# Kernel tuning notes

Measured on AMD Instinct MI355X. Metric: run time of the kernel, lower is better.

## Reference

```python
import jax, jax.numpy as jnp
import numpy as np

B, N, F, UNITS = 8, 2048, 64, 64

def setup_inputs() -> dict:
    key = jax.random.key(0)
    ks = jax.random.split(key, 7)
    inputs = jax.random.normal(ks[0], (B, N, F), dtype=jnp.float32)
    Dynamic_L = jax.random.normal(ks[1], (B, N, N), dtype=jnp.float32)
    W = jax.random.uniform(ks[2], (B, N, N, 3), dtype=jnp.float32)
    Geo = jax.random.normal(ks[3], (N, N), dtype=jnp.float32)
    KL = jax.random.normal(ks[4], (N, N), dtype=jnp.float32)
    # Dense(Units, tanh) params (glorot-ish scale)
    Wd = jax.random.normal(ks[5], (F, UNITS), dtype=jnp.float32) / np.sqrt(F)
    bd = jnp.zeros((UNITS,), dtype=jnp.float32)
    return {"inputs": inputs, "Dynamic_L": Dynamic_L, "W": W,
            "Geo": Geo, "KL": KL, "Wd": Wd, "bd": bd}

def reference(inputs, Dynamic_L, W, Geo, KL, Wd, bd):
    # Weighted fusion of three N x N matrices; Geo/KL broadcast over batch.
    Fusion = Dynamic_L * W[..., 0] + Geo[None] * W[..., 1] + KL[None] * W[..., 2]  # [B,N,N]
    Fusion = jax.nn.softmax(Fusion, axis=-1)
    G1 = jnp.einsum('bnm,bmf->bnf', Fusion, inputs)  # graph matmul [B,N,F]
    return jnp.tanh(G1 @ Wd + bd)  # Dense(Units, tanh) -> [B,N,UNITS]
```

## Files before the change

### kernel.cpp

```cpp
#include <hip/hip_runtime.h>
#include <hip/hip_fp16.h>

#define Nn 2048
#define Ff 64
#define Uu 64
#define NT 512
#define NCH 4
#define G1S 68

typedef _Float16 f16x4 __attribute__((ext_vector_type(4)));
typedef _Float16 f16x8 __attribute__((ext_vector_type(8)));
typedef float    f32x4 __attribute__((ext_vector_type(4)));

#define MFMA32(a,b,c) __builtin_amdgcn_mfma_f32_16x16x32_f16(a,b,c,0,0,0)

#define OWS   65536
#define OINV  65664
#define SMSZ  65792

__global__ __launch_bounds__(256) void transposeX(const float* __restrict__ X,
                                                  _Float16* __restrict__ Xt) {
    __shared__ _Float16 tile[64][65];
    const int b = blockIdx.x, kt = blockIdx.y;
    #pragma unroll
    for (int i = 0; i < 16; ++i) {
        int e  = i * 256 + threadIdx.x;
        int kk = e >> 6, ff = e & 63;
        tile[ff][kk] = (_Float16)X[((size_t)b * Nn + kt * 64 + kk) * Ff + ff];
    }
    __syncthreads();
    #pragma unroll
    for (int i = 0; i < 16; ++i) {
        int e  = i * 256 + threadIdx.x;
        int ff = e >> 6, kk = e & 63;
        Xt[((size_t)b * Ff + ff) * Nn + kt * 64 + kk] = tile[ff][kk];
    }
}

#define ISSUE2(d0v,d1v,gv,kv,w00,w01,w02,w10,w11,w12, C, UR, H) {   \
    const size_t _o = (size_t)(UR) * Nn + ((size_t)(C) << 9)        \
                    + ((H) << 8) + (lane << 2);                     \
    d0v = *(const float4*)(dR0 + _o);                               \
    d1v = *(const float4*)(dR1 + _o);                               \
    gv  = *(const float4*)(gR + _o);                                \
    kv  = *(const float4*)(kR + _o);                                \
    w00 = *(const float4*)(wR0 + 3 * _o);                           \
    w01 = *(const float4*)(wR0 + 3 * _o + 4);                       \
    w02 = *(const float4*)(wR0 + 3 * _o + 8);                       \
    w10 = *(const float4*)(wR1 + 3 * _o);                           \
    w11 = *(const float4*)(wR1 + 3 * _o + 4);                       \
    w12 = *(const float4*)(wR1 + 3 * _o + 8);                       \
}

#define CONSUME2(d0v,d1v,gv,kv,w00,w01,w02,w10,w11,w12, P0B,P1B, UR, H) {       \
    const int _tr = row0 + (UR);                                                \
    float a0 = __expf(fminf(d0v.x*w00.x + gv.x*w00.y + kv.x*w00.z, 11.f));      \
    float a1 = __expf(fminf(d0v.y*w00.w + gv.y*w01.x + kv.y*w01.y, 11.f));      \
    float a2 = __expf(fminf(d0v.z*w01.z + gv.z*w01.w + kv.z*w02.x, 11.f));      \
    float a3 = __expf(fminf(d0v.w*w02.y + gv.w*w02.z + kv.w*w02.w, 11.f));      \
    float c0 = __expf(fminf(d1v.x*w10.x + gv.x*w10.y + kv.x*w10.z, 11.f));      \
    float c1 = __expf(fminf(d1v.y*w10.w + gv.y*w11.x + kv.y*w11.y, 11.f));      \
    float c2 = __expf(fminf(d1v.z*w11.z + gv.z*w11.w + kv.z*w12.x, 11.f));      \
    float c3 = __expf(fminf(d1v.w*w12.y + gv.w*w12.z + kv.w*w12.w, 11.f));      \
    f16x4 h0 = {(_Float16)a0, (_Float16)a1, (_Float16)a2, (_Float16)a3};        \
    f16x4 h1 = {(_Float16)c0, (_Float16)c1, (_Float16)c2, (_Float16)c3};        \
    rs0[UR] += (float)h0[0] + (float)h0[1] + (float)h0[2] + (float)h0[3];       \
    rs1[UR] += (float)h1[0] + (float)h1[1] + (float)h1[2] + (float)h1[3];       \
    const int _ba = (_tr * 1024 + ((H) << 9) + (lane << 3))                     \
                    ^ ((_tr & 7) << 4);                                         \
    *(f16x4*)((P0B) + _ba) = h0;                                                \
    *(f16x4*)((P1B) + _ba) = h1;                                                \
}

#define STAGE_CHUNK2(P0B, P1B, C) {                                              \
    ISSUE2(Ad0,Ad1,Agv,Akv,Aw00,Aw01,Aw02,Aw10,Aw11,Aw12, C, 0, 0);              \
    ISSUE2(Bd0,Bd1,Bgv,Bkv,Bw00,Bw01,Bw02,Bw10,Bw11,Bw12, C, 0, 1);              \
    CONSUME2(Ad0,Ad1,Agv,Akv,Aw00,Aw01,Aw02,Aw10,Aw11,Aw12, P0B,P1B, 0, 0);      \
    ISSUE2(Ad0,Ad1,Agv,Akv,Aw00,Aw01,Aw02,Aw10,Aw11,Aw12, C, 1, 0);              \
    CONSUME2(Bd0,Bd1,Bgv,Bkv,Bw00,Bw01,Bw02,Bw10,Bw11,Bw12, P0B,P1B, 0, 1);      \
    ISSUE2(Bd0,Bd1,Bgv,Bkv,Bw00,Bw01,Bw02,Bw10,Bw11,Bw12, C, 1, 1);              \
    CONSUME2(Ad0,Ad1,Agv,Akv,Aw00,Aw01,Aw02,Aw10,Aw11,Aw12, P0B,P1B, 1, 0);      \
    CONSUME2(Bd0,Bd1,Bgv,Bkv,Bw00,Bw01,Bw02,Bw10,Bw11,Bw12, P0B,P1B, 1, 1);      \
}

#define MFMA_PHASE2(PBUF, XC) {                                               \
    f16x8 p0 = *(const f16x8*)((XC));                                         \
    f16x8 p1 = *(const f16x8*)((XC) + 32);                                    \
    f16x8 p2 = *(const f16x8*)((XC) + 64);                                    \
    f16x8 p3 = *(const f16x8*)((XC) + 96);                                    \
    f16x8 p4 = *(const f16x8*)((XC) + 128);                                   \
    f16x8 p5 = *(const f16x8*)((XC) + 160);                                   \
    f16x8 p6 = *(const f16x8*)((XC) + 192);                                   \
    f16x8 p7 = *(const f16x8*)((XC) + 224);                                   \
    _Pragma("unroll")                                                         \
    for (int kk = 0; kk < 8; ++kk) {                                          \
        const int aa = r * 1024 + kk * 64 + kg * 16;                          \
        f16x8 af = *(const f16x8*)((PBUF) + (aa ^ ((r & 7) << 4)));           \
        f16x8 bv = (kk==0)?p0:(kk==1)?p1:(kk==2)?p2:(kk==3)?p3:               \
                   (kk==4)?p4:(kk==5)?p5:(kk==6)?p6:p7;                       \
        acc = MFMA32(af, bv, acc);                                            \
    }                                                                         \
    p0 = *(const f16x8*)((XC) + 256);                                         \
    p1 = *(const f16x8*)((XC) + 288);                                         \
    p2 = *(const f16x8*)((XC) + 320);                                         \
    p3 = *(const f16x8*)((XC) + 352);                                         \
    p4 = *(const f16x8*)((XC) + 384);                                         \
    p5 = *(const f16x8*)((XC) + 416);                                         \
    p6 = *(const f16x8*)((XC) + 448);                                         \
    p7 = *(const f16x8*)((XC) + 480);                                         \
    _Pragma("unroll")                                                         \
    for (int kk = 0; kk < 8; ++kk) {                                          \
        const int aa = r * 1024 + (kk + 8) * 64 + kg * 16;                    \
        f16x8 af = *(const f16x8*)((PBUF) + (aa ^ ((r & 7) << 4)));           \
        f16x8 bv = (kk==0)?p0:(kk==1)?p1:(kk==2)?p2:(kk==3)?p3:               \
                   (kk==4)?p4:(kk==5)?p5:(kk==6)?p6:p7;                       \
        acc = MFMA32(af, bv, acc);                                            \
    }                                                                         \
}

__global__ __launch_bounds__(NT, 4) void fused_gcn(
    const _Float16* __restrict__ Xt,
    const float* __restrict__ Dyn,
    const float* __restrict__ Wf,
    const float* __restrict__ Geo,
    const float* __restrict__ KLm,
    const float* __restrict__ Wd,
    const float* __restrict__ bdv,
    float* __restrict__ out)
{
    __shared__ __align__(16) char SM[SMSZ];

    const int t    = threadIdx.x;
    const int lane = t & 63;
    const int wid  = t >> 6;
    const int r    = lane & 15;
    const int kg   = lane >> 4;
    const int rg   = blockIdx.x & 127;
    const int pp   = blockIdx.x >> 7;
    const int n0   = rg << 4;
    const int b0   = pp * 2, b1 = pp * 2 + 1;
    const int row0 = wid << 1;

    const float* dR0 = Dyn + ((size_t)b0 * Nn + n0 + row0) * Nn;
    const float* dR1 = Dyn + ((size_t)b1 * Nn + n0 + row0) * Nn;
    const float* wR0 = Wf  + ((size_t)b0 * Nn + n0 + row0) * (size_t)Nn * 3;
    const float* wR1 = Wf  + ((size_t)b1 * Nn + n0 + row0) * (size_t)Nn * 3;
    const float* gR  = Geo + (size_t)(n0 + row0) * Nn;
    const float* kR  = KLm + (size_t)(n0 + row0) * Nn;

    const int bb = wid >> 2, ct = wid & 3;
    const _Float16* xwv = Xt + (size_t)(bb ? b1 : b0) * Ff * Nn
                        + (size_t)(ct * 16 + r) * Nn + (kg << 3);

    f32x4 acc = {0.f,0.f,0.f,0.f};
    float rs0[2] = {0.f,0.f}, rs1[2] = {0.f,0.f};
    float4 Ad0,Ad1,Agv,Akv,Aw00,Aw01,Aw02,Aw10,Aw11,Aw12;
    float4 Bd0,Bd1,Bgv,Bkv,Bw00,Bw01,Bw02,Bw10,Bw11,Bw12;

    STAGE_CHUNK2(SM, SM + 16384, 0);
    __syncthreads();

    #pragma unroll 1
    for (int c = 0; c < NCH; ++c) {
        const char* pb = SM + (c & 1) * 32768 + bb * 16384;
        MFMA_PHASE2(pb, xwv + ((size_t)c << 9));
        if (c + 1 < NCH) {
            char* bufn = SM + ((c + 1) & 1) * 32768;
            STAGE_CHUNK2(bufn, bufn + 16384, c + 1);
        }
        __syncthreads();
    }

    float* ws = (float*)(SM + OWS);
    #pragma unroll
    for (int i = 0; i < 2; ++i) {
        float v = rs0[i];
        v += __shfl_xor(v, 1, 64);  v += __shfl_xor(v, 2, 64);
        v += __shfl_xor(v, 4, 64);  v += __shfl_xor(v, 8, 64);
        v += __shfl_xor(v, 16, 64); v += __shfl_xor(v, 32, 64);
        float u = rs1[i];
        u += __shfl_xor(u, 1, 64);  u += __shfl_xor(u, 2, 64);
        u += __shfl_xor(u, 4, 64);  u += __shfl_xor(u, 8, 64);
        u += __shfl_xor(u, 16, 64); u += __shfl_xor(u, 32, 64);
        if (lane == 0) { ws[row0 + i] = v; ws[16 + row0 + i] = u; }
    }
    __syncthreads();
    float* inv = (float*)(SM + OINV);
    if (t < 32) inv[t] = 1.0f / ws[t];
    __syncthreads();

    float* g1a = (float*)SM;
    float* g1b = (float*)(SM + 4352);
    float* g1w = bb ? g1b : g1a;
    #pragma unroll
    for (int i = 0; i < 4; ++i) {
        const int ro = (kg << 2) + i;
        g1w[ro * G1S + ct * 16 + r] = acc[i] * inv[bb * 16 + ro];
    }
    __syncthreads();

    const int rw0 = (wid & 3) << 2;
    const float* gg = (bb ? g1b : g1a) + rw0 * G1S;
    const int ob = bb ? b1 : b0;
    float bias = bdv[lane];
    float o0 = bias, o1 = bias, o2 = bias, o3 = bias;
    #pragma unroll 4
    for (int f = 0; f < Ff; ++f) {
        float wdv = Wd[f * Uu + lane];
        o0 += gg[f] * wdv;           o1 += gg[G1S + f] * wdv;
        o2 += gg[2 * G1S + f] * wdv; o3 += gg[3 * G1S + f] * wdv;
    }
    float oo[4] = {o0, o1, o2, o3};
    #pragma unroll
    for (int i = 0; i < 4; ++i) {
        float x  = fminf(fmaxf(oo[i], -15.f), 15.f);
        float ex = __expf(2.f * x);
        out[((size_t)ob * Nn + n0 + rw0 + i) * Uu + lane] = (ex - 1.f) / (ex + 1.f);
    }
}

extern "C" void kernel_launch(void* const* d_in, const int* in_sizes, int n_in,
                              void* d_out, int out_size, void* d_ws, size_t ws_size,
                              hipStream_t stream) {
    const float* X   = (const float*)d_in[0];
    const float* Dyn = (const float*)d_in[1];
    const float* Wf  = (const float*)d_in[2];
    const float* Geo = (const float*)d_in[3];
    const float* KLm = (const float*)d_in[4];
    const float* Wd  = (const float*)d_in[5];
    const float* bdv = (const float*)d_in[6];
    float* out = (float*)d_out;

    _Float16* Xt = (_Float16*)d_ws;
    transposeX<<<dim3(8, Nn / 64), dim3(256), 0, stream>>>(X, Xt);
    fused_gcn<<<dim3(4 * 128), dim3(NT), 0, stream>>>(
        Xt, Dyn, Wf, Geo, KLm, Wd, bdv, out);
}
```

Measured before the change: 156.8 us.

## Halve rows per block to 8, shrink LDS, and use 256-thread blocks

Each block now covers 8 output rows per batch pair with 4 waves instead of 16 rows with 8 waves, which doubles the grid to 1024 blocks and roughly halves shared memory. Each wave computes two 16-column MFMA tiles, and rows 8-15 of each 16-row MFMA tile read from a zeroed LDS pad. The intent is higher occupancy and less register pressure during the load-heavy staging phase, with the loads split into separate per-batch A/B issues. The cost is half of each MFMA's work being wasted on zero rows, plus more per-block overhead.

```diff
diff --git a/kernel.cpp b/kernel.cpp
--- a/kernel.cpp
+++ b/kernel.cpp
@@ -4,7 +4,7 @@
 #define Nn 2048
 #define Ff 64
 #define Uu 64
-#define NT 512
+#define NT 256
 #define NCH 4
 #define G1S 68
 
@@ -14,9 +14,12 @@
 
 #define MFMA32(a,b,c) __builtin_amdgcn_mfma_f32_16x16x32_f16(a,b,c,0,0,0)
 
-#define OWS   65536
-#define OINV  65664
-#define SMSZ  65792
+#define OPB  0
+#define OZB  32768
+#define OWS  32896
+#define OINV 32960
+#define OG1  33024
+#define SMSZ 37376
 
 __global__ __launch_bounds__(256) void transposeX(const float* __restrict__ X,
                                                   _Float16* __restrict__ Xt) {
@@ -37,53 +40,69 @@
     }
 }
 
-#define ISSUE2(d0v,d1v,gv,kv,w00,w01,w02,w10,w11,w12, C, UR, H) {   \
+#define ISSUEA(C, UR, H) {                                          \
     const size_t _o = (size_t)(UR) * Nn + ((size_t)(C) << 9)        \
                     + ((H) << 8) + (lane << 2);                     \
-    d0v = *(const float4*)(dR0 + _o);                               \
-    d1v = *(const float4*)(dR1 + _o);                               \
-    gv  = *(const float4*)(gR + _o);                                \
-    kv  = *(const float4*)(kR + _o);                                \
-    w00 = *(const float4*)(wR0 + 3 * _o);                           \
-    w01 = *(const float4*)(wR0 + 3 * _o + 4);                       \
-    w02 = *(const float4*)(wR0 + 3 * _o + 8);                       \
-    w10 = *(const float4*)(wR1 + 3 * _o);                           \
-    w11 = *(const float4*)(wR1 + 3 * _o + 4);                       \
-    w12 = *(const float4*)(wR1 + 3 * _o + 8);                       \
-}
-
-#define CONSUME2(d0v,d1v,gv,kv,w00,w01,w02,w10,w11,w12, P0B,P1B, UR, H) {       \
+    Ad  = *(const float4*)(dR0 + _o);                               \
+    Aw0 = *(const float4*)(wR0 + 3 * _o);                           \
+    Aw1 = *(const float4*)(wR0 + 3 * _o + 4);                       \
+    Aw2 = *(const float4*)(wR0 + 3 * _o + 8);                       \
+    Ag  = *(const float4*)(gR + _o);                                \
+    Ak  = *(const float4*)(kR + _o);                                \
+}
+#define ISSUEB(C, UR, H) {                                          \
+    const size_t _o = (size_t)(UR) * Nn + ((size_t)(C) << 9)        \
+                    + ((H) << 8) + (lane << 2);                     \
+    Bd  = *(const float4*)(dR1 + _o);                               \
+    Bw0 = *(const float4*)(wR1 + 3 * _o);                           \
+    Bw1 = *(const float4*)(wR1 + 3 * _o + 4);                       \
+    Bw2 = *(const float4*)(wR1 + 3 * _o + 8);                       \
+}
+
+#define CONSUMEA(P0B, UR, H) {                                                  \
     const int _tr = row0 + (UR);                                                \
-    float a0 = __expf(fminf(d0v.x*w00.x + gv.x*w00.y + kv.x*w00.z, 11.f));      \
-    float a1 = __expf(fminf(d0v.y*w00.w + gv.y*w01.x + kv.y*w01.y, 11.f));      \
-    float a2 = __expf(fminf(d0v.z*w01.z + gv.z*w01.w + kv.z*w02.x, 11.f));      \
-    float a3 = __expf(fminf(d0v.w*w02.y + gv.w*w02.z + kv.w*w02.w, 11.f));      \
-    float c0 = __expf(fminf(d1v.x*w10.x + gv.x*w10.y + kv.x*w10.z, 11.f));      \
-    float c1 = __expf(fminf(d1v.y*w10.w + gv.y*w11.x + kv.y*w11.y, 11.f));      \
-    float c2 = __expf(fminf(d1v.z*w11.z + gv.z*w11.w + kv.z*w12.x, 11.f));      \
-    float c3 = __expf(fminf(d1v.w*w12.y + gv.w*w12.z + kv.w*w12.w, 11.f));      \
-    f16x4 h0 = {(_Float16)a0, (_Float16)a1, (_Float16)a2, (_Float16)a3};        \
-    f16x4 h1 = {(_Float16)c0, (_Float16)c1, (_Float16)c2, (_Float16)c3};        \
-    rs0[UR] += (float)h0[0] + (float)h0[1] + (float)h0[2] + (float)h0[3];       \
-    rs1[UR] += (float)h1[0] + (float)h1[1] + (float)h1[2] + (float)h1[3];       \
-    const int _ba = (_tr * 1024 + ((H) << 9) + (lane << 3))                     \
-                    ^ ((_tr & 7) << 4);                                         \
-    *(f16x4*)((P0B) + _ba) = h0;                                                \
-    *(f16x4*)((P1B) + _ba) = h1;                                                \
-}
-
-#define STAGE_CHUNK2(P0B, P1B, C) {                                              \
-    ISSUE2(Ad0,Ad1,Agv,Akv,Aw00,Aw01,Aw02,Aw10,Aw11,Aw12, C, 0, 0);              \
-    ISSUE2(Bd0,Bd1,Bgv,Bkv,Bw00,Bw01,Bw02,Bw10,Bw11,Bw12, C, 0, 1);              \
-    CONSUME2(Ad0,Ad1,Agv,Akv,Aw00,Aw01,Aw02,Aw10,Aw11,Aw12, P0B,P1B, 0, 0);      \
-    ISSUE2(Ad0,Ad1,Agv,Akv,Aw00,Aw01,Aw02,Aw10,Aw11,Aw12, C, 1, 0);              \
-    CONSUME2(Bd0,Bd1,Bgv,Bkv,Bw00,Bw01,Bw02,Bw10,Bw11,Bw12, P0B,P1B, 0, 1);      \
-    ISSUE2(Bd0,Bd1,Bgv,Bkv,Bw00,Bw01,Bw02,Bw10,Bw11,Bw12, C, 1, 1);              \
-    CONSUME2(Ad0,Ad1,Agv,Akv,Aw00,Aw01,Aw02,Aw10,Aw11,Aw12, P0B,P1B, 1, 0);      \
-    CONSUME2(Bd0,Bd1,Bgv,Bkv,Bw00,Bw01,Bw02,Bw10,Bw11,Bw12, P0B,P1B, 1, 1);      \
-}
-
-#define MFMA_PHASE2(PBUF, XC) {                                               \
+    float e0 = __expf(fminf(Ad.x*Aw0.x + Ag.x*Aw0.y + Ak.x*Aw0.z, 11.f));       \
+    float e1 = __expf(fminf(Ad.y*Aw0.w + Ag.y*Aw1.x + Ak.y*Aw1.y, 11.f));       \
+    float e2 = __expf(fminf(Ad.z*Aw1.z + Ag.z*Aw1.w + Ak.z*Aw2.x, 11.f));       \
+    float e3 = __expf(fminf(Ad.w*Aw2.y + Ag.w*Aw2.z + Ak.w*Aw2.w, 11.f));       \
+    f16x4 h = {(_Float16)e0, (_Float16)e1, (_Float16)e2, (_Float16)e3};         \
+    rs0[UR] += (float)h[0] + (float)h[1] + (float)h[2] + (float)h[3];           \
+    const int _ba = (_tr * 1024 + ((H) << 9) + (lane << 3)) ^ ((_tr & 7) << 4); \
+    *(f16x4*)((P0B) + _ba) = h;                                                 \
+    gC = Ag; kC = Ak;          \
+}
+#define CONSUMEB(P1B, UR, H) {                                                  \
+    const int _tr = row0 + (UR);                                                \
+    float e0 = __expf(fminf(Bd.x*Bw0.x + gC.x*Bw0.y + kC.x*Bw0.z, 11.f));       \
+    float e1 = __expf(fminf(Bd.y*Bw0.w + gC.y*Bw1.x + kC.y*Bw1.y, 11.f));       \
+    float e2 = __expf(fminf(Bd.z*Bw1.z + gC.z*Bw1.w + kC.z*Bw2.x, 11.f));       \
+    float e3 = __expf(fminf(Bd.w*Bw2.y + gC.w*Bw2.z + kC.w*Bw2.w, 11.f));       \
+    f16x4 h = {(_Float16)e0, (_Float16)e1, (_Float16)e2, (_Float16)e3};         \
+    rs1[UR] += (float)h[0] + (float)h[1] + (float)h[2] + (float)h[3];           \
+    const int _ba = (_tr * 1024 + ((H) << 9) + (lane << 3)) ^ ((_tr & 7) << 4); \
+    *(f16x4*)((P1B) + _ba) = h;                                                 \
+}
+
+#define STAGE_CHUNK(P0B, P1B, C) {        \
+    ISSUEA(C, 0, 0);                      \
+    ISSUEB(C, 0, 0);                      \
+    CONSUMEA(P0B, 0, 0);                  \
+    ISSUEA(C, 0, 1);                      \
+    CONSUMEB(P1B, 0, 0);                  \
+    ISSUEB(C, 0, 1);                      \
+    CONSUMEA(P0B, 0, 1);                  \
+    ISSUEA(C, 1, 0);                      \
+    CONSUMEB(P1B, 0, 1);                  \
+    ISSUEB(C, 1, 0);                      \
+    CONSUMEA(P0B, 1, 0);                  \
+    ISSUEA(C, 1, 1);                      \
+    CONSUMEB(P1B, 1, 0);                  \
+    ISSUEB(C, 1, 1);                      \
+    CONSUMEA(P0B, 1, 1);                  \
+    CONSUMEB(P1B, 1, 1);                  \
+}
+
+#define MFMA_TILE(PBUF, XC, ACC) {                                            \
     f16x8 p0 = *(const f16x8*)((XC));                                         \
     f16x8 p1 = *(const f16x8*)((XC) + 32);                                    \
     f16x8 p2 = *(const f16x8*)((XC) + 64);                                    \
@@ -94,11 +113,12 @@
     f16x8 p7 = *(const f16x8*)((XC) + 224);                                   \
     _Pragma("unroll")                                                         \
     for (int kk = 0; kk < 8; ++kk) {                                          \
-        const int aa = r * 1024 + kk * 64 + kg * 16;                          \
-        f16x8 af = *(const f16x8*)((PBUF) + (aa ^ ((r & 7) << 4)));           \
+        const int aa = (r * 1024 + kk * 64 + kg * 16) ^ ((r & 7) << 4);       \
+        const char* ap = (r < 8) ? ((PBUF) + aa) : zp;                        \
+        f16x8 af = *(const f16x8*)ap;                                         \
         f16x8 bv = (kk==0)?p0:(kk==1)?p1:(kk==2)?p2:(kk==3)?p3:               \
                    (kk==4)?p4:(kk==5)?p5:(kk==6)?p6:p7;                       \
-        acc = MFMA32(af, bv, acc);                                            \
+        ACC = MFMA32(af, bv, ACC);                                            \
     }                                                                         \
     p0 = *(const f16x8*)((XC) + 256);                                         \
     p1 = *(const f16x8*)((XC) + 288);                                         \
@@ -110,11 +130,12 @@
     p7 = *(const f16x8*)((XC) + 480);                                         \
     _Pragma("unroll")                                                         \
     for (int kk = 0; kk < 8; ++kk) {                                          \
-        const int aa = r * 1024 + (kk + 8) * 64 + kg * 16;                    \
-        f16x8 af = *(const f16x8*)((PBUF) + (aa ^ ((r & 7) << 4)));           \
+        const int aa = (r * 1024 + (kk + 8) * 64 + kg * 16) ^ ((r & 7) << 4); \
+        const char* ap = (r < 8) ? ((PBUF) + aa) : zp;                        \
+        f16x8 af = *(const f16x8*)ap;                                         \
         f16x8 bv = (kk==0)?p0:(kk==1)?p1:(kk==2)?p2:(kk==3)?p3:               \
                    (kk==4)?p4:(kk==5)?p5:(kk==6)?p6:p7;                       \
-        acc = MFMA32(af, bv, acc);                                            \
+        ACC = MFMA32(af, bv, ACC);                                            \
     }                                                                         \
 }
 
@@ -135,9 +156,9 @@
     const int wid  = t >> 6;
     const int r    = lane & 15;
     const int kg   = lane >> 4;
-    const int rg   = blockIdx.x & 127;
-    const int pp   = blockIdx.x >> 7;
-    const int n0   = rg << 4;
+    const int rg   = blockIdx.x & 255;
+    const int pp   = blockIdx.x >> 8;
+    const int n0   = rg << 3;
     const int b0   = pp * 2, b1 = pp * 2 + 1;
     const int row0 = wid << 1;
 
@@ -148,25 +169,32 @@
     const float* gR  = Geo + (size_t)(n0 + row0) * Nn;
     const float* kR  = KLm + (size_t)(n0 + row0) * Nn;
 
-    const int bb = wid >> 2, ct = wid & 3;
-    const _Float16* xwv = Xt + (size_t)(bb ? b1 : b0) * Ff * Nn
-                        + (size_t)(ct * 16 + r) * Nn + (kg << 3);
-
-    f32x4 acc = {0.f,0.f,0.f,0.f};
+    const int bb = wid >> 1;
+    const int tA = (wid & 1) << 1;
+    const int bsel = bb ? b1 : b0;
+    const _Float16* xwA = Xt + (size_t)bsel * Ff * Nn
+                        + (size_t)(tA * 16 + r) * Nn + (kg << 3);
+    const _Float16* xwB = xwA + (size_t)16 * Nn;
+    const char* zp = SM + OZB + kg * 16;
+
+    f32x4 accA = {0.f,0.f,0.f,0.f}, accB = {0.f,0.f,0.f,0.f};
     float rs0[2] = {0.f,0.f}, rs1[2] = {0.f,0.f};
-    float4 Ad0,Ad1,Agv,Akv,Aw00,Aw01,Aw02,Aw10,Aw11,Aw12;
-    float4 Bd0,Bd1,Bgv,Bkv,Bw00,Bw01,Bw02,Bw10,Bw11,Bw12;
-
-    STAGE_CHUNK2(SM, SM + 16384, 0);
+    float4 Ad, Aw0, Aw1, Aw2, Ag, Ak;
+    float4 Bd, Bw0, Bw1, Bw2;
+    float4 gC, kC;
+
+    if (t < 32) ((int*)(SM + OZB))[t] = 0;
+    STAGE_CHUNK(SM + OPB, SM + OPB + 8192, 0);
     __syncthreads();
 
     #pragma unroll 1
     for (int c = 0; c < NCH; ++c) {
-        const char* pb = SM + (c & 1) * 32768 + bb * 16384;
-        MFMA_PHASE2(pb, xwv + ((size_t)c << 9));
+        const char* pb = SM + OPB + (c & 1) * 16384 + bb * 8192;
+        MFMA_TILE(pb, xwA + ((size_t)c << 9), accA);
+        MFMA_TILE(pb, xwB + ((size_t)c << 9), accB);
         if (c + 1 < NCH) {
-            char* bufn = SM + ((c + 1) & 1) * 32768;
-            STAGE_CHUNK2(bufn, bufn + 16384, c + 1);
+            char* bn = SM + OPB + ((c + 1) & 1) * 16384;
+            STAGE_CHUNK(bn, bn + 8192, c + 1);
         }
         __syncthreads();
     }
@@ -182,26 +210,29 @@
         u += __shfl_xor(u, 1, 64);  u += __shfl_xor(u, 2, 64);
         u += __shfl_xor(u, 4, 64);  u += __shfl_xor(u, 8, 64);
         u += __shfl_xor(u, 16, 64); u += __shfl_xor(u, 32, 64);
-        if (lane == 0) { ws[row0 + i] = v; ws[16 + row0 + i] = u; }
+        if (lane == 0) { ws[row0 + i] = v; ws[8 + row0 + i] = u; }
     }
     __syncthreads();
     float* inv = (float*)(SM + OINV);
-    if (t < 32) inv[t] = 1.0f / ws[t];
-    __syncthreads();
-
-    float* g1a = (float*)SM;
-    float* g1b = (float*)(SM + 4352);
+    if (t < 16) inv[t] = 1.0f / ws[t];
+    __syncthreads();
+
+    float* g1a = (float*)(SM + OG1);
+    float* g1b = g1a + 8 * G1S;
     float* g1w = bb ? g1b : g1a;
+    const float* invb = inv + bb * 8;
     #pragma unroll
     for (int i = 0; i < 4; ++i) {
         const int ro = (kg << 2) + i;
-        g1w[ro * G1S + ct * 16 + r] = acc[i] * inv[bb * 16 + ro];
-    }
-    __syncthreads();
-
-    const int rw0 = (wid & 3) << 2;
+        if (ro < 8) {
+            g1w[ro * G1S + tA * 16 + r]        = accA[i] * invb[ro];
+            g1w[ro * G1S + (tA + 1) * 16 + r]  = accB[i] * invb[ro];
+        }
+    }
+    __syncthreads();
+
+    const int rw0 = (wid & 1) << 2;
     const float* gg = (bb ? g1b : g1a) + rw0 * G1S;
-    const int ob = bb ? b1 : b0;
     float bias = bdv[lane];
     float o0 = bias, o1 = bias, o2 = bias, o3 = bias;
     #pragma unroll 4
@@ -215,7 +246,7 @@
     for (int i = 0; i < 4; ++i) {
         float x  = fminf(fmaxf(oo[i], -15.f), 15.f);
         float ex = __expf(2.f * x);
-        out[((size_t)ob * Nn + n0 + rw0 + i) * Uu + lane] = (ex - 1.f) / (ex + 1.f);
+        out[((size_t)bsel * Nn + n0 + rw0 + i) * Uu + lane] = (ex - 1.f) / (ex + 1.f);
     }
 }
 
@@ -233,6 +264,6 @@
 
     _Float16* Xt = (_Float16*)d_ws;
     transposeX<<<dim3(8, Nn / 64), dim3(256), 0, stream>>>(X, Xt);
-    fused_gcn<<<dim3(4 * 128), dim3(NT), 0, stream>>>(
+    fused_gcn<<<dim3(256 * 4), dim3(NT), 0, stream>>>(
         Xt, Dyn, Wf, Geo, KLm, Wd, bdv, out);
 }
```

Measured after the change: 163.8 us. 1.04x slower.
